# Performance work log

Hardware: AMD Instinct MI355X
Metric: run time of the kernel (lower is better)

Reference implementation:

```python
import jax, jax.numpy as jnp
import numpy as np

B, T, F = 2048, 128, 128
H, L, K = 512, 8, 10  # hidden_dim, levels, conv_size
CHUNK = H // L
GATES = 4 * H + 2 * L


def setup_inputs() -> dict:
    key = jax.random.key(0)
    ks = jax.random.split(key, 12)
    s_k = 1.0 / np.sqrt(F + 1)
    s_r = 1.0 / np.sqrt(H + 1)
    s_s = 1.0 / np.sqrt(H)
    s_rs = 1.0 / np.sqrt(H // 6)
    s_c = 1.0 / np.sqrt(H * K)
    return {
        'x': jax.random.normal(ks[0], (B, T, F), jnp.float32),
        'time': jax.random.uniform(ks[1], (B, T), jnp.float32),
        'Wk': jax.random.normal(ks[2], (F + 1, GATES), jnp.float32) * s_k,
        'bk': jnp.zeros((GATES,), jnp.float32),
        'Wr': jax.random.normal(ks[3], (H + 1, GATES), jnp.float32) * s_r,
        'br': jnp.zeros((GATES,), jnp.float32),
        'Ws': jax.random.normal(ks[4], (H, H // 6), jnp.float32) * s_s,
        'bs': jax.random.normal(ks[5], (H // 6,), jnp.float32) * 0.01,
        'Wrs': jax.random.normal(ks[6], (H // 6, H), jnp.float32) * s_rs,
        'brs': jax.random.normal(ks[7], (H,), jnp.float32) * 0.01,
        'conv_w': jax.random.normal(ks[8], (H, H, K), jnp.float32) * s_c,  # [out_ch, in_ch, k]
        'conv_b': jax.random.normal(ks[9], (H,), jnp.float32) * 0.01,
    }


def _cumax_l2r(z):
    return jnp.cumsum(jax.nn.softmax(z, axis=-1), axis=-1)


def _cumax_r2l(z):
    return jnp.flip(jnp.cumsum(jax.nn.softmax(jnp.flip(z, -1), axis=-1), axis=-1), -1)


def _phase_forward(x, time, Wk, bk, Wr, br, Ws, bs, Wrs, brs, conv_w, conv_b):
    def step(carry, xs):
        c, h, tmp_h, tmp_dis = carry
        xt, dt = xs
        dt = dt[:, None]
        xo = (jnp.concatenate([xt, dt], -1) @ Wk + bk
              + jnp.concatenate([h, dt], -1) @ Wr + br)  # [B, 4H+2L]
        fm = _cumax_l2r(xo[:, :L])[:, :, None]        # [B, L, 1]
        im = _cumax_r2l(xo[:, L:2 * L])[:, :, None]   # [B, L, 1]
        g = xo[:, 2 * L:].reshape(-1, 4 * L, CHUNK)
        f = jax.nn.sigmoid(g[:, :L])
        i = jax.nn.sigmoid(g[:, L:2 * L])
        o = jax.nn.sigmoid(g[:, 2 * L:3 * L])
        c_in = jnp.tanh(g[:, 3 * L:])
        c_last = c.reshape(-1, L, CHUNK)
        ov = fm * im
        c_new = ov * (f * c_last + i * c_in) + (fm - ov) * c_last + (im - ov) * c_in
        h_new = (o * jnp.tanh(c_new)).reshape(-1, H)
        dist = 1.0 - jnp.mean(fm[..., 0], axis=-1)   # [B]
        tmp_h = jnp.concatenate([tmp_h[1:], h_new[None]], 0)
        tmp_dis = jnp.concatenate([tmp_dis[1:], dist[None]], 0)
        return (c_new.reshape(-1, H), h_new, tmp_h, tmp_dis), dist

    init = (jnp.zeros((B, H), x.dtype), jnp.zeros((B, H), x.dtype),
            jnp.zeros((K, B, H), x.dtype), jnp.zeros((K, B), x.dtype))
    (_, _, tmp_h, tmp_dis), distance = jax.lax.scan(
        step, init, (jnp.transpose(x, (1, 0, 2)), time.T))

    local_dis = jax.nn.softmax(jnp.cumsum(tmp_dis.T, axis=1), axis=1)   # [B, K]
    local_h = jnp.transpose(tmp_h, (1, 2, 0)) * local_dis[:, None, :]   # [B, H, K]
    theme = jax.nn.sigmoid(
        jnp.maximum(jnp.mean(local_h, axis=-1) @ Ws + bs, 0.0) @ Wrs + brs)  # [B, H]
    conv_out = jnp.einsum('bhk,ohk->bo', local_h, conv_w) + conv_b      # valid conv, out len 1
    return theme * conv_out, distance


def reference(x, time, Wk, bk, Wr, br, Ws, bs, Wrs, brs, conv_w, conv_b):
    return _phase_forward(x, time, Wk, bk, Wr, br, Ws, bs, Wrs, brs, conv_w, conv_b)
```

## Files before the change

kernel.cpp:

```cpp
#include <hip/hip_runtime.h>
#include <hip/hip_bf16.h>
#include <cstddef>
#include <cstdint>

namespace {

constexpr int B = 2048, T = 128, F = 128, H = 512, L = 8, KW = 10;
constexpr int GATES = 2064;
constexpr int NG = 2048;
constexpr int KIN = 640;
constexpr int HS = 85;
constexpr int RC = H * KW;
constexpr int KS = 8;
constexpr int NROW = 144;

constexpr int BRES = 16384;
constexpr int BROT = 126976;
constexpr int DTSO = 154624;
constexpr int SMEM_SZ = 155136;

typedef __attribute__((ext_vector_type(8))) short short8;
typedef __attribute__((ext_vector_type(4))) float f32x4;
typedef unsigned long long ull;

__device__ __forceinline__ float fsigmoid_(float x) {
    return __builtin_amdgcn_rcpf(1.0f + __expf(-x));
}
__device__ __forceinline__ float ftanh_(float x) {
    return 1.0f - 2.0f * __builtin_amdgcn_rcpf(1.0f + __expf(2.0f * x));
}

__device__ __forceinline__ void gl_lds16(const void* g, void* l) {
    __builtin_amdgcn_global_load_lds(
        (const __attribute__((address_space(1))) unsigned int*)g,
        (__attribute__((address_space(3))) unsigned int*)l,
        16, 0, 0);
}

__device__ __forceinline__ ull h_atomic_load(const void* p) {
    return __hip_atomic_load((const ull*)p, __ATOMIC_RELAXED, __HIP_MEMORY_SCOPE_AGENT);
}

__global__ __launch_bounds__(256) void prep_wgt(
    const float* __restrict__ Wk, const float* __restrict__ Wr,
    __hip_bfloat16* __restrict__ WgT)
{
    __shared__ float tile[64 * 65];
    const int tid = threadIdx.x;
    const int c0 = blockIdx.x * 64, k0 = blockIdx.y * 64;
#pragma unroll
    for (int rep = 0; rep < 16; ++rep) {
        int e = rep * 256 + tid;
        int kl = e >> 6, cl = e & 63;
        int col = c0 + cl;
        int nt = col >> 7, cc = col & 127;
        int n = 16 + ((cc >> 4) & 3) * 512 + nt * 32 + ((cc >> 6) & 1) * 16 + (cc & 15);
        int k = k0 + kl;
        tile[kl * 65 + cl] = (k < F) ? Wk[(size_t)k * GATES + n] : Wr[(size_t)(k - F) * GATES + n];
    }
    __syncthreads();
    const int cl = tid >> 2, q = tid & 3;
    unsigned short buf[16];
#pragma unroll
    for (int i = 0; i < 16; ++i) {
        float f = tile[(q * 16 + i) * 65 + cl];
        __hip_bfloat16 bv = __float2bfloat16(f);
        buf[i] = *(unsigned short*)&bv;
    }
    int col = c0 + cl;
    int nt = col >> 7, rin = col & 127;
    unsigned short* dst = (unsigned short*)WgT + (size_t)nt * NROW * KIN + (size_t)rin * KIN + k0 + q * 16;
    *(short8*)dst = *(short8*)&buf[0];
    *(short8*)(dst + 8) = *(short8*)&buf[8];
}

__global__ void prep_w16rep(const float* __restrict__ Wk, const float* __restrict__ Wr,
                            __hip_bfloat16* __restrict__ WgT)
{
    int idx = blockIdx.x * blockDim.x + threadIdx.x;
    if (idx >= 16 * 16 * KIN) return;
    int nt = idx / (16 * KIN);
    int rem = idx % (16 * KIN);
    int n = rem / KIN, k = rem % KIN;
    float v = (k < F) ? Wk[(size_t)k * GATES + n] : Wr[(size_t)(k - F) * GATES + n];
    WgT[(size_t)nt * NROW * KIN + (size_t)(128 + n) * KIN + k] = __float2bfloat16(v);
}

__global__ void prep_small(const float* __restrict__ Wk, const float* __restrict__ bk,
                           const float* __restrict__ Wr, const float* __restrict__ br,
                           float* __restrict__ biasg, float* __restrict__ wrowg,
                           float* __restrict__ bias16, float* __restrict__ wrow16)
{
    const int total = 2 * NG + 32;
    for (int idx = threadIdx.x; idx < total; idx += 256) {
        if (idx < NG) {
            int col = idx;
            int nt = col >> 7, cc = col & 127;
            int n = 16 + ((cc >> 4) & 3) * 512 + nt * 32 + ((cc >> 6) & 1) * 16 + (cc & 15);
            biasg[col] = bk[n] + br[n];
        } else if (idx < 2 * NG) {
            int col = idx - NG;
            int nt = col >> 7, cc = col & 127;
            int n = 16 + ((cc >> 4) & 3) * 512 + nt * 32 + ((cc >> 6) & 1) * 16 + (cc & 15);
            wrowg[col] = Wk[(size_t)F * GATES + n] + Wr[(size_t)H * GATES + n];
        } else if (idx < 2 * NG + 16) {
            int n = idx - 2 * NG;
            bias16[n] = bk[n] + br[n];
        } else {
            int n = idx - 2 * NG - 16;
            wrow16[n] = Wk[(size_t)F * GATES + n] + Wr[(size_t)H * GATES + n];
        }
    }
}

__global__ void convert_x(const float* __restrict__ x, __hip_bfloat16* __restrict__ xb) {
    int i = blockIdx.x * blockDim.x + threadIdx.x;
    size_t o = (size_t)i * 4;
    if (o >= (size_t)B * T * F) return;
    float4 v = *(const float4*)(x + o);
    xb[o + 0] = __float2bfloat16(v.x);
    xb[o + 1] = __float2bfloat16(v.y);
    xb[o + 2] = __float2bfloat16(v.z);
    xb[o + 3] = __float2bfloat16(v.w);
}

__global__ void prep_convw(const float* __restrict__ conv_w, __hip_bfloat16* __restrict__ CWb) {
    int i = blockIdx.x * blockDim.x + threadIdx.x;
    if (i >= H * RC / 4) return;
    size_t o = (size_t)i * 4;
    float4 v = *(const float4*)(conv_w + o);
    CWb[o + 0] = __float2bfloat16(v.x);
    CWb[o + 1] = __float2bfloat16(v.y);
    CWb[o + 2] = __float2bfloat16(v.z);
    CWb[o + 3] = __float2bfloat16(v.w);
}

__global__ __launch_bounds__(256) void prep_tmet(const float* __restrict__ tin,
                                                 float* __restrict__ tout)
{
    __shared__ float tl[32][33];
    const int bb = blockIdx.x * 32, tt = blockIdx.y * 32;
    const int tx = threadIdx.x & 31, ty = threadIdx.x >> 5;
#pragma unroll
    for (int r = 0; r < 32; r += 8)
        tl[ty + r][tx] = tin[(size_t)(bb + ty + r) * T + tt + tx];
    __syncthreads();
#pragma unroll
    for (int r = 0; r < 32; r += 8)
        tout[(size_t)(tt + ty + r) * B + bb + tx] = tl[tx][ty + r];
}

struct StepArgs {
    const __hip_bfloat16* xb;
    __hip_bfloat16* h0;
    __hip_bfloat16* h1;
    const __hip_bfloat16* WgT;
    const float* biasg;
    const float* wrowg;
    const float* bias16;
    const float* wrow16;
    const float* tmeT;
    __hip_bfloat16* tmp_h;
    float* tmp_ds;
    float* dist_out;
    unsigned* bar;
};

__global__ __launch_bounds__(512, 2) void persistent_step(StepArgs a)
{
    __shared__ __align__(16) char smem[SMEM_SZ];
    float* logitS = (float*)smem;
    float* fmimS = (float*)(smem + BROT);
    unsigned short* hstageS = (unsigned short*)(smem + 135168);
    float* dts = (float*)(smem + DTSO);

    const int tid = threadIdx.x;
    const int wave = tid >> 6;
    const int wr = wave >> 1, wc = wave & 1;
    const int quad = (tid & 63) >> 4, m16 = tid & 15;
    const int l = blockIdx.x;
    const int nt = ((l & 7) << 1) | ((l >> 3) & 1);
    const int mt = l >> 4;
    const int m0 = mt * 128;
    const int lidx = nt >> 1;

    const int o0 = tid * 16;
    const int arow = o0 >> 6;
    const int asl = ((((o0 >> 4) & 3) ^ ((arow >> 1) & 3)) << 3);
    const char* xbT = (const char*)a.xb + (size_t)(m0 + arow) * (T * F * 2) + asl * 2;
    const size_t hbyte = (size_t)(m0 + arow) * (H * 2) + asl * 2;
    const unsigned short* wgt_tile = (const unsigned short*)a.WgT + (size_t)nt * NROW * KIN;
    const int brow0 = o0 >> 6;
    const int bsl0 = ((((o0 >> 4) & 3) ^ ((brow0 >> 1) & 3)) << 3);
    const char* bsT0 = (const char*)(wgt_tile + (size_t)brow0 * KIN + bsl0);
    const int ob1 = 8192 + tid * 16;
    const int brow1 = ob1 >> 6;
    const int bsl1 = ((((ob1 >> 4) & 3) ^ ((brow1 >> 1) & 3)) << 3);
    const char* bsT1 = (const char*)(wgt_tile + (size_t)brow1 * KIN + bsl1);
    const bool bv1 = (tid < 64);

    auto stageB = [&](int s, int bufbyte) {
        gl_lds16(bsT0 + s * 64, smem + bufbyte + o0);
        if (bv1) gl_lds16(bsT1 + s * 64, smem + bufbyte + ob1);
    };

    const int hcol = nt * 32 + wc * 16 + m16;
    float bj[4], wj[4];
#pragma unroll
    for (int j = 0; j < 4; ++j) {
        int col = nt * 128 + wc * 64 + j * 16 + m16;
        bj[j] = a.biasg[col];
        wj[j] = a.wrowg[col];
    }
    const int soff = (tid >= 128 && tid < 256) ? 8 : 0;
    float b16r8[8], w16r8[8];
#pragma unroll
    for (int n = 0; n < 8; ++n) { b16r8[n] = a.bias16[soff + n]; w16r8[n] = a.wrow16[soff + n]; }

    const unsigned short* Abase = (const unsigned short*)smem;
    const unsigned short* Bbase = (const unsigned short*)(smem + BROT);

    float creg[2][4] = {};
    ull areg[2][2];

    {
#pragma unroll
        for (int s = 0; s < 12; ++s) stageB(s, BRES + s * 9216);
        gl_lds16(xbT, smem + o0);
        stageB(12, BROT + 0 * 9216);
        stageB(13, BROT + 1 * 9216);
        areg[1][0] = h_atomic_load(xbT + 64);  areg[1][1] = h_atomic_load(xbT + 72);
        areg[0][0] = h_atomic_load(xbT + 128); areg[0][1] = h_atomic_load(xbT + 136);
    }
    __syncthreads();

#pragma unroll 1
    for (int t = 0; t < T; ++t) {
        const char* xt = xbT + (size_t)t * 256;
        const char* hs = (const char*)((t & 1) ? a.h1 : a.h0) + hbyte;
        unsigned* hout32 = (unsigned*)((t & 1) ? a.h0 : a.h1);

        float dtreg = 0.f;
        if (tid < 128) dtreg = a.tmeT[(size_t)t * B + m0 + tid];

        f32x4 acc[2][4] = {};
        f32x4 acc16[2] = {};

#pragma unroll
        for (int ki = 0; ki < 20; ++ki) {
            if (ki > 0) {
                if (ki <= 13) {
                    asm volatile("s_waitcnt lgkmcnt(0)" ::: "memory");
                } else if (ki <= 17) {
                    if (bv1) asm volatile("s_waitcnt vmcnt(6) lgkmcnt(0)" ::: "memory");
                    else     asm volatile("s_waitcnt vmcnt(5) lgkmcnt(0)" ::: "memory");
                } else if (ki == 18) {
                    if (bv1) asm volatile("s_waitcnt vmcnt(4) lgkmcnt(0)" ::: "memory");
                    else     asm volatile("s_waitcnt vmcnt(3) lgkmcnt(0)" ::: "memory");
                } else {
                    asm volatile("s_waitcnt vmcnt(0) lgkmcnt(0)" ::: "memory");
                }
                __builtin_amdgcn_s_barrier();
                __builtin_amdgcn_sched_barrier(0);
            }
            const int nxt = ki + 1;
            if (nxt < 20) {
                char* adst = smem + (nxt & 1) * 8192 + o0;
                *(ull*)adst = areg[nxt & 1][0];
                *(ull*)(adst + 8) = areg[nxt & 1][1];
            }
            if (ki >= 12 && ki <= 17) {
                const int s = ki + 2;
                stageB(s, BROT + ((s - 12) % 3) * 9216);
            }
            __builtin_amdgcn_sched_barrier(0);
            const int fut = ki + 3;
            if (fut < 20) {
                if (fut <= 3) {
                    areg[fut & 1][0] = h_atomic_load(xt + fut * 64);
                    areg[fut & 1][1] = h_atomic_load(xt + fut * 64 + 8);
                } else {
                    areg[fut & 1][0] = h_atomic_load(hs + fut * 64 - 256);
                    areg[fut & 1][1] = h_atomic_load(hs + fut * 64 - 248);
                }
            }
            __builtin_amdgcn_sched_barrier(0);
            const unsigned short* A = Abase + (ki & 1) * 4096;
            const unsigned short* Bb = (const unsigned short*)
                (smem + (ki < 12 ? BRES + ki * 9216 : BROT + ((ki - 12) % 3) * 9216));
            short8 av[2], bv[4];
#pragma unroll
            for (int i = 0; i < 2; ++i) {
                int ar = wr * 32 + i * 16 + m16;
                av[i] = *(const short8*)&A[ar * 32 + ((quad ^ ((ar >> 1) & 3)) << 3)];
            }
#pragma unroll
            for (int j = 0; j < 4; ++j) {
                int br = wc * 64 + j * 16 + m16;
                bv[j] = *(const short8*)&Bb[br * 32 + ((quad ^ ((br >> 1) & 3)) << 3)];
            }
#pragma unroll
            for (int i = 0; i < 2; ++i)
#pragma unroll
                for (int j = 0; j < 4; ++j)
                    acc[i][j] = __builtin_amdgcn_mfma_f32_16x16x32_bf16(av[i], bv[j], acc[i][j], 0, 0, 0);
            if (wc == 0) {
                int lr = 128 + m16;
                short8 wv = *(const short8*)&Bb[lr * 32 + ((quad ^ ((lr >> 1) & 3)) << 3)];
                acc16[0] = __builtin_amdgcn_mfma_f32_16x16x32_bf16(av[0], wv, acc16[0], 0, 0, 0);
                acc16[1] = __builtin_amdgcn_mfma_f32_16x16x32_bf16(av[1], wv, acc16[1], 0, 0, 0);
            }
        }
        __syncthreads();

        if (tid < 128) dts[tid] = dtreg;
        if (wc == 0) {
#pragma unroll
            for (int i = 0; i < 2; ++i)
#pragma unroll
                for (int r = 0; r < 4; ++r)
                    logitS[(wr * 32 + i * 16 + quad * 4 + r) * 17 + m16] = acc16[i][r];
        }
        __syncthreads();

        if (tid < 256) {
            const int row = tid & 127;
            const int m = m0 + row;
            const bool hi = tid >= 128;
            const float dt = hi ? dts[row] : dtreg;
            float z[8];
#pragma unroll
            for (int n = 0; n < 8; ++n)
                z[n] = logitS[row * 17 + soff + n] + b16r8[n] + dt * w16r8[n];
            float mx = z[0];
#pragma unroll
            for (int j = 1; j < 8; ++j) mx = fmaxf(mx, z[j]);
            float e[8], s = 0.f;
#pragma unroll
            for (int j = 0; j < 8; ++j) { e[j] = __expf(z[j] - mx); s += e[j]; }
            const float inv = __builtin_amdgcn_rcpf(s);
            if (!hi) {
                float run = 0.f, fsum = 0.f, val = 0.f;
#pragma unroll
                for (int j = 0; j < 8; ++j) {
                    run += e[j];
                    float fmv = run * inv;
                    if (j == lidx) val = fmv;
                    fsum += fmv;
                }
                fmimS[row * 2] = val;
                if (nt == 0) {
                    float d = 1.0f - fsum * 0.125f;
                    a.dist_out[(size_t)t * B + m] = d;
                    if (t >= T - KW) a.tmp_ds[(size_t)(t - (T - KW)) * B + m] = d;
                }
            } else {
                float run = 0.f, val = 0.f;
#pragma unroll
                for (int j = 7; j >= 0; --j) {
                    run += e[j];
                    if (j == lidx) val = run * inv;
                }
                fmimS[row * 2 + 1] = val;
            }
        }
        __syncthreads();

#pragma unroll
        for (int i = 0; i < 2; ++i) {
#pragma unroll
            for (int r = 0; r < 4; ++r) {
                int rl = wr * 32 + i * 16 + quad * 4 + r;
                int m = m0 + rl;
                float dt = dts[rl];
                float fmv = fmimS[rl * 2];
                float imv = fmimS[rl * 2 + 1];
                float fg = fsigmoid_(acc[i][0][r] + bj[0] + dt * wj[0]);
                float ig = fsigmoid_(acc[i][1][r] + bj[1] + dt * wj[1]);
                float og = fsigmoid_(acc[i][2][r] + bj[2] + dt * wj[2]);
                float ci = ftanh_(acc[i][3][r] + bj[3] + dt * wj[3]);
                float ov = fmv * imv;
                float cl = creg[i][r];
                float cn = ov * (fg * cl + ig * ci) + (fmv - ov) * cl + (imv - ov) * ci;
                float hn = og * ftanh_(cn);
                creg[i][r] = cn;
                __hip_bfloat16 hb = __float2bfloat16(hn);
                hstageS[rl * 32 + (wc * 16 + m16)] = *(unsigned short*)&hb;
                if (t >= T - KW) a.tmp_h[((size_t)(t - (T - KW)) * B + m) * H + hcol] = hb;
            }
        }
        __syncthreads();

        {
            const unsigned* hs32 = (const unsigned*)hstageS;
#pragma unroll
            for (int wds = 0; wds < 4; ++wds) {
                int wi = wds * 512 + tid;
                int row = wi >> 4, cp = wi & 15;
                unsigned v = hs32[row * 16 + cp];
                __hip_atomic_store(hout32 + (size_t)(m0 + row) * (H / 2) + nt * 16 + cp, v,
                                   __ATOMIC_RELAXED, __HIP_MEMORY_SCOPE_AGENT);
            }
        }

        __syncthreads();
        if (t != T - 1) {
            const char* xn = xbT + (size_t)(t + 1) * 256;
            gl_lds16(xn, smem + o0);
            stageB(12, BROT + 0 * 9216);
            stageB(13, BROT + 1 * 9216);
            areg[1][0] = h_atomic_load(xn + 64);  areg[1][1] = h_atomic_load(xn + 72);
            areg[0][0] = h_atomic_load(xn + 128); areg[0][1] = h_atomic_load(xn + 136);
            if (tid == 0) {
                unsigned* ctr = a.bar + (mt << 6);
                __hip_atomic_fetch_add(ctr, 1u, __ATOMIC_RELAXED, __HIP_MEMORY_SCOPE_AGENT);
                const unsigned tgt = 16u * (unsigned)(t + 1);
                for (int it = 0; it < (1 << 22); ++it) {
                    if (__hip_atomic_load(ctr, __ATOMIC_RELAXED, __HIP_MEMORY_SCOPE_AGENT) >= tgt) break;
                    __builtin_amdgcn_s_sleep(2);
                }
            }
            __syncthreads();
        }
    }
}

__global__ __launch_bounds__(128) void post_local(
    const __hip_bfloat16* __restrict__ tmp_h, const float* __restrict__ tmp_dis,
    float* __restrict__ mean_h, __hip_bfloat16* __restrict__ Ahk)
{
    const int b = blockIdx.x;
    const int tid = threadIdx.x;
    __shared__ float ld[KW];
    if (tid == 0) {
        float cd[KW];
        float run = 0.f;
        for (int k = 0; k < KW; ++k) { run += tmp_dis[(size_t)k * B + b]; cd[k] = run; }
        float mx = cd[0];
        for (int k = 1; k < KW; ++k) mx = fmaxf(mx, cd[k]);
        float s = 0.f;
        for (int k = 0; k < KW; ++k) { cd[k] = expf(cd[k] - mx); s += cd[k]; }
        for (int k = 0; k < KW; ++k) ld[k] = cd[k] / s;
    }
    __syncthreads();
    float ldr[KW];
#pragma unroll
    for (int k = 0; k < KW; ++k) ldr[k] = ld[k];
    for (int h = tid; h < H; h += 128) {
        float s = 0.f;
#pragma unroll
        for (int k = 0; k < KW; ++k) {
            float v = __bfloat162float(tmp_h[((size_t)k * B + b) * H + h]) * ldr[k];
            s += v;
            Ahk[(size_t)b * RC + h * KW + k] = __float2bfloat16(v);
        }
        mean_h[(size_t)b * H + h] = s * (1.0f / KW);
    }
}

__global__ void theme1_k(const float* __restrict__ mean_h, const float* __restrict__ Ws,
                         const float* __restrict__ bs, float* __restrict__ t1)
{
    int idx = blockIdx.x * blockDim.x + threadIdx.x;
    if (idx >= B * HS) return;
    int b = idx / HS, j = idx % HS;
    float s = bs[j];
    const float* mh = mean_h + (size_t)b * H;
    for (int h = 0; h < H; ++h) s += mh[h] * Ws[(size_t)h * HS + j];
    t1[idx] = fmaxf(s, 0.f);
}

__global__ void theme2_k(const float* __restrict__ t1, const float* __restrict__ Wrs,
                         const float* __restrict__ brs, float* __restrict__ theme)
{
    int idx = blockIdx.x * blockDim.x + threadIdx.x;
    if (idx >= B * H) return;
    int b = idx / H, o = idx % H;
    float s = brs[o];
    const float* tv = t1 + (size_t)b * HS;
    for (int j = 0; j < HS; ++j) s += tv[j] * Wrs[(size_t)j * H + o];
    theme[idx] = 1.0f / (1.0f + expf(-s));
}

__global__ __launch_bounds__(256) void conv_split(
    const __hip_bfloat16* __restrict__ Ahk, const __hip_bfloat16* __restrict__ CWb,
    float* __restrict__ Pbuf)
{
    __shared__ __align__(16) unsigned short As2[128 * 64];
    __shared__ __align__(16) unsigned short Bs2[128 * 64];
    const int tid = threadIdx.x;
    const int wave = tid >> 6;
    const int wr = wave >> 1, wc = wave & 1;
    const int quad = (tid & 63) >> 4, m16 = tid & 15;
    const int n0 = blockIdx.x * 128, m0 = blockIdx.y * 128;
    const int ksb = blockIdx.z * (RC / KS);

    f32x4 acc[4][4] = {};
    for (int k0 = 0; k0 < RC / KS; k0 += 64) {
#pragma unroll
        for (int p = 0; p < 4; ++p) {
            int o = p * 4096 + tid * 16;
            int row = o >> 7, slot = (o >> 4) & 7;
            int kg = ksb + k0 + (slot ^ (row & 7)) * 8;
            gl_lds16((const unsigned short*)Ahk + (size_t)(m0 + row) * RC + kg, (char*)As2 + o);
            gl_lds16((const unsigned short*)CWb + (size_t)(n0 + row) * RC + kg, (char*)Bs2 + o);
        }
        __syncthreads();
#pragma unroll
        for (int c2 = 0; c2 < 2; ++c2) {
            const int k8 = c2 * 4 + quad;
            short8 av[4], bv[4];
#pragma unroll
            for (int i = 0; i < 4; ++i) {
                int arow2 = wr * 64 + i * 16 + m16;
                av[i] = *(const short8*)&As2[arow2 * 64 + (k8 ^ (arow2 & 7)) * 8];
            }
#pragma unroll
            for (int j = 0; j < 4; ++j) {
                int brow = wc * 64 + j * 16 + m16;
                bv[j] = *(const short8*)&Bs2[brow * 64 + (k8 ^ (brow & 7)) * 8];
            }
#pragma unroll
            for (int i = 0; i < 4; ++i)
#pragma unroll
                for (int j = 0; j < 4; ++j)
                    acc[i][j] = __builtin_amdgcn_mfma_f32_16x16x32_bf16(av[i], bv[j], acc[i][j], 0, 0, 0);
        }
        __syncthreads();
    }
    float* P = Pbuf + (size_t)blockIdx.z * B * H;
#pragma unroll
    for (int j = 0; j < 4; ++j) {
        const int col = n0 + wc * 64 + j * 16 + m16;
#pragma unroll
        for (int i = 0; i < 4; ++i) {
            const int rb = m0 + wr * 64 + i * 16 + quad * 4;
#pragma unroll
            for (int r = 0; r < 4; ++r)
                P[(size_t)(rb + r) * H + col] = acc[i][j][r];
        }
    }
}

__global__ void conv_reduce(const float* __restrict__ Pbuf, const float* __restrict__ conv_b,
                            const float* __restrict__ theme, float* __restrict__ out0)
{
    int i = blockIdx.x * blockDim.x + threadIdx.x;
    if (i >= B * H) return;
    float s = conv_b[i & (H - 1)];
#pragma unroll
    for (int ks = 0; ks < KS; ++ks) s += Pbuf[(size_t)ks * B * H + i];
    out0[i] = theme[i] * s;
}

}

extern "C" void kernel_launch(void* const* d_in, const int* in_sizes, int n_in,
                              void* d_out, int out_size, void* d_ws, size_t ws_size,
                              hipStream_t stream)
{
    (void)in_sizes; (void)n_in; (void)out_size; (void)ws_size;
    const float* x      = (const float*)d_in[0];
    const float* tme    = (const float*)d_in[1];
    const float* Wk     = (const float*)d_in[2];
    const float* bk     = (const float*)d_in[3];
    const float* Wr     = (const float*)d_in[4];
    const float* br     = (const float*)d_in[5];
    const float* Ws     = (const float*)d_in[6];
    const float* bs     = (const float*)d_in[7];
    const float* Wrs    = (const float*)d_in[8];
    const float* brs    = (const float*)d_in[9];
    const float* conv_w = (const float*)d_in[10];
    const float* conv_b = (const float*)d_in[11];

    float* out0 = (float*)d_out;
    float* dist_out = out0 + (size_t)B * H;

    char* w = (char*)d_ws;
    __hip_bfloat16* WgT  = (__hip_bfloat16*)w; w += (size_t)16 * NROW * KIN * 2;
    __hip_bfloat16* xb   = (__hip_bfloat16*)w; w += (size_t)B * T * F * 2;
    __hip_bfloat16* CWb  = (__hip_bfloat16*)w; w += (size_t)H * RC * 2;
    __hip_bfloat16* Ahk  = (__hip_bfloat16*)w; w += (size_t)B * RC * 2;
    __hip_bfloat16* hb0  = (__hip_bfloat16*)w; w += (size_t)B * H * 2;
    __hip_bfloat16* hb1  = (__hip_bfloat16*)w; w += (size_t)B * H * 2;
    __hip_bfloat16* tmp_h = (__hip_bfloat16*)w; w += (size_t)KW * B * H * 2;
    float* biasg  = (float*)w; w += (size_t)NG * 4;
    float* wrowg  = (float*)w; w += (size_t)NG * 4;
    float* bias16 = (float*)w; w += 64;
    float* wrow16 = (float*)w; w += 64;
    float* tmp_ds = (float*)w; w += (size_t)KW * B * 4;
    float* mean_h = (float*)w; w += (size_t)B * H * 4;
    float* t1     = (float*)w; w += (size_t)B * HS * 4;
    float* theme  = (float*)w; w += (size_t)B * H * 4;
    float* Pbuf   = (float*)w; w += (size_t)KS * B * H * 4;
    float* tmeT   = (float*)w; w += (size_t)T * B * 4;
    unsigned* bar = (unsigned*)w; w += 4096;

    hipMemsetAsync(hb0, 0, (size_t)B * H * sizeof(__hip_bfloat16), stream);
    hipMemsetAsync(bar, 0, 4096, stream);

    prep_wgt<<<dim3(NG / 64, KIN / 64), 256, 0, stream>>>(Wk, Wr, WgT);
    prep_w16rep<<<(16 * 16 * KIN + 255) / 256, 256, 0, stream>>>(Wk, Wr, WgT);
    prep_small<<<1, 256, 0, stream>>>(Wk, bk, Wr, br, biasg, wrowg, bias16, wrow16);
    convert_x<<<((B * T * F / 4) + 255) / 256, 256, 0, stream>>>(x, xb);
    prep_convw<<<((H * RC / 4) + 255) / 256, 256, 0, stream>>>(conv_w, CWb);
    prep_tmet<<<dim3(B / 32, T / 32), 256, 0, stream>>>(tme, tmeT);

    {
        StepArgs sa;
        sa.xb = xb; sa.h0 = hb0; sa.h1 = hb1; sa.WgT = WgT;
        sa.biasg = biasg; sa.wrowg = wrowg; sa.bias16 = bias16; sa.wrow16 = wrow16;
        sa.tmeT = tmeT; sa.tmp_h = tmp_h; sa.tmp_ds = tmp_ds; sa.dist_out = dist_out;
        sa.bar = bar;
        persistent_step<<<256, 512, 0, stream>>>(sa);
    }

    post_local<<<B, 128, 0, stream>>>(tmp_h, tmp_ds, mean_h, Ahk);
    theme1_k<<<(B * HS + 255) / 256, 256, 0, stream>>>(mean_h, Ws, bs, t1);
    theme2_k<<<(B * H + 255) / 256, 256, 0, stream>>>(t1, Wrs, brs, theme);
    conv_split<<<dim3(H / 128, B / 128, KS), 256, 0, stream>>>(Ahk, CWb, Pbuf);
    conv_reduce<<<(B * H + 255) / 256, 256, 0, stream>>>(Pbuf, conv_b, theme, out0);
}
```

Measured before the change: 1.744 ms.

## Deepen A/B LDS ring to four slots and halve per-k barriers

Restructures the per-step GEMM k-loop pipeline. The A operand now uses a 4-slot LDS ring with the x tiles staged directly by global_load_lds, and the streamed weight tiles use a 4-slot ring starting earlier (10 resident instead of 12). Barriers happen only every second k-step, which cuts sync overhead at the cost of more LDS and fewer resident weights. The grid barrier arrival is also moved before the next-step prefetch, so other blocks see the arrival sooner.

```diff
diff --git a/kernel.cpp b/kernel.cpp
--- a/kernel.cpp
+++ b/kernel.cpp
@@ -14,10 +14,13 @@
 constexpr int KS = 8;
 constexpr int NROW = 144;
 
-constexpr int BRES = 16384;
-constexpr int BROT = 126976;
-constexpr int DTSO = 154624;
-constexpr int SMEM_SZ = 155136;
+constexpr int BRES = 32768;
+constexpr int BRING = 124928;
+constexpr int DTSO = 161792;
+constexpr int LOGO  = 0;
+constexpr int FMIMO = 124928;
+constexpr int HSTO  = 125952;
+constexpr int SMEM_SZ = 162304;
 
 typedef __attribute__((ext_vector_type(8))) short short8;
 typedef __attribute__((ext_vector_type(4))) float f32x4;
@@ -169,9 +172,9 @@
 __global__ __launch_bounds__(512, 2) void persistent_step(StepArgs a)
 {
     __shared__ __align__(16) char smem[SMEM_SZ];
-    float* logitS = (float*)smem;
-    float* fmimS = (float*)(smem + BROT);
-    unsigned short* hstageS = (unsigned short*)(smem + 135168);
+    float* logitS = (float*)(smem + LOGO);
+    float* fmimS = (float*)(smem + FMIMO);
+    unsigned short* hstageS = (unsigned short*)(smem + HSTO);
     float* dts = (float*)(smem + DTSO);
 
     const int tid = threadIdx.x;
@@ -218,25 +221,22 @@
     for (int n = 0; n < 8; ++n) { b16r8[n] = a.bias16[soff + n]; w16r8[n] = a.wrow16[soff + n]; }
 
     const unsigned short* Abase = (const unsigned short*)smem;
-    const unsigned short* Bbase = (const unsigned short*)(smem + BROT);
 
     float creg[2][4] = {};
     ull areg[2][2];
 
     {
 #pragma unroll
-        for (int s = 0; s < 12; ++s) stageB(s, BRES + s * 9216);
+        for (int s = 0; s < 10; ++s) stageB(s, BRES + s * 9216);
         gl_lds16(xbT, smem + o0);
-        stageB(12, BROT + 0 * 9216);
-        stageB(13, BROT + 1 * 9216);
-        areg[1][0] = h_atomic_load(xbT + 64);  areg[1][1] = h_atomic_load(xbT + 72);
+        gl_lds16(xbT + 64, smem + 8192 + o0);
         areg[0][0] = h_atomic_load(xbT + 128); areg[0][1] = h_atomic_load(xbT + 136);
+        areg[1][0] = h_atomic_load(xbT + 192); areg[1][1] = h_atomic_load(xbT + 200);
     }
     __syncthreads();
 
 #pragma unroll 1
     for (int t = 0; t < T; ++t) {
-        const char* xt = xbT + (size_t)t * 256;
         const char* hs = (const char*)((t & 1) ? a.h1 : a.h0) + hbyte;
         unsigned* hout32 = (unsigned*)((t & 1) ? a.h0 : a.h1);
 
@@ -248,46 +248,34 @@
 
 #pragma unroll
         for (int ki = 0; ki < 20; ++ki) {
-            if (ki > 0) {
-                if (ki <= 13) {
+            if (ki > 0 && (ki & 1) == 0) {
+                if (ki <= 8)
                     asm volatile("s_waitcnt lgkmcnt(0)" ::: "memory");
-                } else if (ki <= 17) {
-                    if (bv1) asm volatile("s_waitcnt vmcnt(6) lgkmcnt(0)" ::: "memory");
-                    else     asm volatile("s_waitcnt vmcnt(5) lgkmcnt(0)" ::: "memory");
-                } else if (ki == 18) {
-                    if (bv1) asm volatile("s_waitcnt vmcnt(4) lgkmcnt(0)" ::: "memory");
-                    else     asm volatile("s_waitcnt vmcnt(3) lgkmcnt(0)" ::: "memory");
-                } else {
+                else if (ki <= 16)
+                    asm volatile("s_waitcnt vmcnt(2) lgkmcnt(0)" ::: "memory");
+                else
                     asm volatile("s_waitcnt vmcnt(0) lgkmcnt(0)" ::: "memory");
-                }
                 __builtin_amdgcn_s_barrier();
                 __builtin_amdgcn_sched_barrier(0);
             }
-            const int nxt = ki + 1;
-            if (nxt < 20) {
-                char* adst = smem + (nxt & 1) * 8192 + o0;
-                *(ull*)adst = areg[nxt & 1][0];
-                *(ull*)(adst + 8) = areg[nxt & 1][1];
-            }
-            if (ki >= 12 && ki <= 17) {
-                const int s = ki + 2;
-                stageB(s, BROT + ((s - 12) % 3) * 9216);
+            if (ki < 18) {
+                char* adst = smem + ((ki + 2) & 3) * 8192 + o0;
+                *(ull*)adst = areg[ki & 1][0];
+                *(ull*)(adst + 8) = areg[ki & 1][1];
+            }
+            if (ki >= 8 && ki <= 17) {
+                stageB(ki + 2, BRING + ((ki - 8) & 3) * 9216);
             }
             __builtin_amdgcn_sched_barrier(0);
-            const int fut = ki + 3;
-            if (fut < 20) {
-                if (fut <= 3) {
-                    areg[fut & 1][0] = h_atomic_load(xt + fut * 64);
-                    areg[fut & 1][1] = h_atomic_load(xt + fut * 64 + 8);
-                } else {
-                    areg[fut & 1][0] = h_atomic_load(hs + fut * 64 - 256);
-                    areg[fut & 1][1] = h_atomic_load(hs + fut * 64 - 248);
-                }
+            if (ki <= 15) {
+                const size_t ko = (size_t)(ki + 4) * 64 - 256;
+                areg[ki & 1][0] = h_atomic_load(hs + ko);
+                areg[ki & 1][1] = h_atomic_load(hs + ko + 8);
             }
             __builtin_amdgcn_sched_barrier(0);
-            const unsigned short* A = Abase + (ki & 1) * 4096;
+            const unsigned short* A = Abase + (ki & 3) * 4096;
             const unsigned short* Bb = (const unsigned short*)
-                (smem + (ki < 12 ? BRES + ki * 9216 : BROT + ((ki - 12) % 3) * 9216));
+                (smem + (ki < 10 ? BRES + ki * 9216 : BRING + ((ki - 10) & 3) * 9216));
             short8 av[2], bv[4];
 #pragma unroll
             for (int i = 0; i < 2; ++i) {
@@ -405,15 +393,15 @@
 
         __syncthreads();
         if (t != T - 1) {
+            unsigned* ctr = a.bar + (mt << 6);
+            if (tid == 0)
+                __hip_atomic_fetch_add(ctr, 1u, __ATOMIC_RELAXED, __HIP_MEMORY_SCOPE_AGENT);
             const char* xn = xbT + (size_t)(t + 1) * 256;
             gl_lds16(xn, smem + o0);
-            stageB(12, BROT + 0 * 9216);
-            stageB(13, BROT + 1 * 9216);
-            areg[1][0] = h_atomic_load(xn + 64);  areg[1][1] = h_atomic_load(xn + 72);
+            gl_lds16(xn + 64, smem + 8192 + o0);
             areg[0][0] = h_atomic_load(xn + 128); areg[0][1] = h_atomic_load(xn + 136);
+            areg[1][0] = h_atomic_load(xn + 192); areg[1][1] = h_atomic_load(xn + 200);
             if (tid == 0) {
-                unsigned* ctr = a.bar + (mt << 6);
-                __hip_atomic_fetch_add(ctr, 1u, __ATOMIC_RELAXED, __HIP_MEMORY_SCOPE_AGENT);
                 const unsigned tgt = 16u * (unsigned)(t + 1);
                 for (int it = 0; it < (1 << 22); ++it) {
                     if (__hip_atomic_load(ctr, __ATOMIC_RELAXED, __HIP_MEMORY_SCOPE_AGENT) >= tgt) break;
```

Measured after the change: 1.808 ms. +3.7%, slower.
